# Kernel optimization log

Measured on AMD Instinct MI355X. Metric: run time of the kernel, lower is better.

The kernel has to match this reference:

```python
import jax, jax.numpy as jnp
import numpy as np

N_NODES = 50000
N_EDGES = 600000
IN_DIM = 128
HID_DIM = 128
OUT_DIM = 128
N_GRAPHS = 64


def _glorot(key, shape):
    lim = np.sqrt(6.0 / (shape[0] + shape[1]))
    return jax.random.uniform(key, shape, jnp.float32, -lim, lim)


def setup_inputs() -> dict:
    key = jax.random.key(0)
    ks = jax.random.split(key, 8)
    h = jax.random.normal(ks[0], (N_NODES, IN_DIM), jnp.float32)
    src = jax.random.randint(ks[1], (N_EDGES,), 0, N_NODES, jnp.int64)
    dst = jax.random.randint(ks[2], (N_EDGES,), 0, N_NODES, jnp.int64)
    graph_ids = jnp.sort(jax.random.randint(ks[3], (N_NODES,), 0, N_GRAPHS, jnp.int64))
    W1 = _glorot(ks[4], (IN_DIM, HID_DIM)); b1 = jnp.zeros((HID_DIM,), jnp.float32)
    W2 = _glorot(ks[5], (HID_DIM, HID_DIM)); b2 = jnp.zeros((HID_DIM,), jnp.float32)
    W3 = _glorot(ks[6], (HID_DIM, OUT_DIM)); b3 = jnp.zeros((OUT_DIM,), jnp.float32)
    return {"h": h, "src": src, "dst": dst, "graph_ids": graph_ids,
            "W1": W1, "b1": b1, "W2": W2, "b2": b2, "W3": W3, "b3": b3,
            "n_graphs": N_GRAPHS}


def _graph_conv(h, src, dst, norm_src, norm_dst, W, b):
    # DGL GraphConv, norm='both': D_dst^{-1/2} A^T D_src^{-1/2} h W + b
    m = h * norm_src[:, None]                                   # [N, d]
    agg = jax.ops.segment_sum(m[src], dst, num_segments=h.shape[0])  # [N, d]
    return (agg * norm_dst[:, None]) @ W + b


def reference(h, src, dst, graph_ids, W1, b1, W2, b2, W3, b3, n_graphs):
    n = h.shape[0]
    ones = jnp.ones((src.shape[0],), h.dtype)
    out_deg = jnp.clip(jax.ops.segment_sum(ones, src, num_segments=n), 1.0)
    in_deg = jnp.clip(jax.ops.segment_sum(ones, dst, num_segments=n), 1.0)
    norm_src = out_deg ** -0.5
    norm_dst = in_deg ** -0.5

    x = jax.nn.relu(_graph_conv(h, src, dst, norm_src, norm_dst, W1, b1))
    x = jax.nn.relu(_graph_conv(x, src, dst, norm_src, norm_dst, W2, b2))
    x = jax.nn.relu(_graph_conv(x, src, dst, norm_src, norm_dst, W3, b3))

    # dgl.mean_nodes: per-graph mean over nodes
    gsum = jax.ops.segment_sum(x, graph_ids, num_segments=n_graphs)          # [G, d]
    gcnt = jax.ops.segment_sum(jnp.ones((n,), x.dtype), graph_ids, num_segments=n_graphs)
    return gsum / jnp.clip(gcnt, 1.0)[:, None]
```

## Files before the change

kernel.cpp:

```cpp
#include <hip/hip_runtime.h>
#include <hip/hip_fp16.h>


#define DIM 128

typedef _Float16 half8 __attribute__((ext_vector_type(8)));
typedef float floatx4 __attribute__((ext_vector_type(4)));

#define HIST_R 4
#define HIST_S 64
#define NPR 12500
#define LDSW (NPR / 2)

__global__ __launch_bounds__(256) void k_hist(const int* __restrict__ src,
                                              const int* __restrict__ dst,
                                              unsigned* __restrict__ partial, int E) {
    __shared__ unsigned hist[LDSW];
    int b = blockIdx.x;
    int a = b / (HIST_R * HIST_S);
    int r = (b / HIST_S) % HIST_R;
    int s = b % HIST_S;
    const int* arr = a ? dst : src;
    for (int i = threadIdx.x; i < LDSW; i += 256) hist[i] = 0;
    __syncthreads();
    int chunk = (E + HIST_S - 1) / HIST_S;
    int e0 = s * chunk;
    int e1 = min(e0 + chunk, E);
    unsigned base = (unsigned)(r * NPR);
    for (int i = e0 + threadIdx.x; i < e1; i += 256) {
        unsigned n = (unsigned)arr[i] - base;
        if (n < NPR) atomicAdd(&hist[n >> 1], 1u << ((n & 1) * 16));
    }
    __syncthreads();
    unsigned* outp = partial + ((size_t)(a * HIST_R + r) * HIST_S + s) * LDSW;
    for (int i = threadIdx.x; i < LDSW; i += 256) outp[i] = hist[i];
}

__global__ void k_hist_merge(const unsigned* __restrict__ partial,
                             float* __restrict__ ns, float* __restrict__ nd,
                             int* __restrict__ inc, int N) {
    int t = blockIdx.x * blockDim.x + threadIdx.x;
    const int total_w = HIST_R * LDSW;
    if (t >= 2 * total_w) return;
    int a = t / total_w;
    int wg = t % total_w;
    int r = wg / LDSW;
    int w = wg % LDSW;
    const unsigned* p = partial + ((size_t)(a * HIST_R + r) * HIST_S) * LDSW + w;
    unsigned sum = 0;
#pragma unroll
    for (int s = 0; s < HIST_S; ++s) sum += p[(size_t)s * LDSW];
    int n0 = r * NPR + w * 2;
    int d0 = (int)(sum & 0xFFFFu);
    int d1 = (int)(sum >> 16);
    if (a == 0) {
        if (n0 < N)     ns[n0]     = rsqrtf(fmaxf((float)d0, 1.0f));
        if (n0 + 1 < N) ns[n0 + 1] = rsqrtf(fmaxf((float)d1, 1.0f));
    } else {
        if (n0 < N)     { nd[n0]     = rsqrtf(fmaxf((float)d0, 1.0f)); inc[n0]     = d0; }
        if (n0 + 1 < N) { nd[n0 + 1] = rsqrtf(fmaxf((float)d1, 1.0f)); inc[n0 + 1] = d1; }
    }
}

__global__ void k_scan_partial(const int* __restrict__ inc, int* __restrict__ bsum, int N) {
    __shared__ int s[256];
    int i = blockIdx.x * 256 + threadIdx.x;
    int t = threadIdx.x;
    s[t] = (i < N) ? inc[i] : 0;
    __syncthreads();
    for (int off = 128; off > 0; off >>= 1) {
        if (t < off) s[t] += s[t + off];
        __syncthreads();
    }
    if (t == 0) bsum[blockIdx.x] = s[0];
}

__global__ void k_scan_top(int* __restrict__ bsum, int nb) {
    __shared__ int s[256];
    int t = threadIdx.x;
    int v = (t < nb) ? bsum[t] : 0;
    s[t] = v;
    __syncthreads();
    for (int off = 1; off < 256; off <<= 1) {
        int u = (t >= off) ? s[t - off] : 0;
        __syncthreads();
        s[t] += u;
        __syncthreads();
    }
    if (t < nb) bsum[t] = s[t] - v;
}

__global__ void k_scan_write(const int* __restrict__ inc, const int* __restrict__ bsum,
                             int* __restrict__ row_ptr, int N) {
    __shared__ int s[256];
    int i = blockIdx.x * 256 + threadIdx.x;
    int t = threadIdx.x;
    int v = (i < N) ? inc[i] : 0;
    s[t] = v;
    __syncthreads();
    for (int off = 1; off < 256; off <<= 1) {
        int u = (t >= off) ? s[t - off] : 0;
        __syncthreads();
        s[t] += u;
        __syncthreads();
    }
    int ex = bsum[blockIdx.x] + s[t] - v;
    if (i < N) row_ptr[i] = ex;
    if (i == N - 1) row_ptr[N] = ex + v;
}

__global__ void k_cursor(const unsigned* __restrict__ partial, const int* __restrict__ row_ptr,
                         int* __restrict__ cur, int N) {
    int t = blockIdx.x * blockDim.x + threadIdx.x;
    if (t >= HIST_R * LDSW) return;
    int r = t / LDSW;
    int w = t % LDSW;
    int n0 = r * NPR + 2 * w;
    const unsigned* p = partial + ((size_t)(HIST_R + r) * HIST_S) * LDSW + w;
    int run0 = (n0 < N) ? row_ptr[n0] : 0;
    int run1 = (n0 + 1 < N) ? row_ptr[n0 + 1] : 0;
    int* c = cur + (size_t)r * HIST_S * NPR + 2 * w;
#pragma unroll
    for (int s = 0; s < HIST_S; ++s) {
        c[(size_t)s * NPR + 0] = run0;
        c[(size_t)s * NPR + 1] = run1;
        unsigned hv = p[(size_t)s * LDSW];
        run0 += (int)(hv & 0xFFFFu);
        run1 += (int)(hv >> 16);
    }
}

__global__ __launch_bounds__(256) void k_fill2(const int* __restrict__ src,
                                               const int* __restrict__ dst,
                                               const int* __restrict__ cur,
                                               int* __restrict__ csr, int E) {
    __shared__ int lcur[NPR];
    int r = blockIdx.x / HIST_S;
    int s = blockIdx.x % HIST_S;
    const int* cs = cur + (size_t)(r * HIST_S + s) * NPR;
    for (int i = threadIdx.x; i < NPR; i += 256) lcur[i] = cs[i];
    __syncthreads();
    int chunk = (E + HIST_S - 1) / HIST_S;
    int e0 = s * chunk;
    int e1 = min(e0 + chunk, E);
    unsigned base = (unsigned)(r * NPR);
    for (int i = e0 + threadIdx.x; i < e1; i += 256) {
        unsigned d = (unsigned)dst[i] - base;
        if (d < NPR) {
            int p = atomicAdd(&lcur[d], 1);
            csr[p] = src[i];
        }
    }
}

__global__ void k_h2half(const float4* __restrict__ h, const float* __restrict__ ns,
                         uint2* __restrict__ A, int N) {
    int i = blockIdx.x * blockDim.x + threadIdx.x;
    if (i < N * 32) {
        int n = i >> 5;
        float s = ns[n];
        float4 v = h[i];
        __half2 p0 = __floats2half2_rn(v.x * s, v.y * s);
        __half2 p1 = __floats2half2_rn(v.z * s, v.w * s);
        uint2 o;
        o.x = *(unsigned*)&p0;
        o.y = *(unsigned*)&p1;
        A[i] = o;
    }
}

__global__ void k_w2half(const float* __restrict__ W, _Float16* __restrict__ Wt) {
    int i = blockIdx.x * blockDim.x + threadIdx.x;
    int k = i >> 7;
    int n = i & 127;
    Wt[(size_t)n * DIM + k] = (_Float16)W[i];
}

__global__ void k_agg(const uint2* __restrict__ A, const int* __restrict__ row_ptr,
                      const int* __restrict__ csr, const float* __restrict__ nd,
                      uint2* __restrict__ Bh, int N) {
    int gtid = blockIdx.x * blockDim.x + threadIdx.x;
    int node = gtid >> 6;
    int lane = threadIdx.x & 63;
    if (node >= N) return;
    int e0 = row_ptr[node];
    int e1 = row_ptr[node + 1];
    int half = lane >> 5;
    int l8 = lane & 31;
    float ax = 0.f, ay = 0.f, az = 0.f, aw = 0.f;

    auto acc4 = [&](uint2 u) {
        __half2 p0 = *(__half2*)&u.x;
        __half2 p1 = *(__half2*)&u.y;
        float2 f0 = __half22float2(p0);
        float2 f1 = __half22float2(p1);
        ax += f0.x; ay += f0.y; az += f1.x; aw += f1.y;
    };

    int e = e0;
    for (; e + 8 <= e1; e += 8) {
        int s0 = csr[e + half];
        int s1 = csr[e + 2 + half];
        int s2 = csr[e + 4 + half];
        int s3 = csr[e + 6 + half];
        uint2 u0 = A[(size_t)s0 * 32 + l8];
        uint2 u1 = A[(size_t)s1 * 32 + l8];
        uint2 u2 = A[(size_t)s2 * 32 + l8];
        uint2 u3 = A[(size_t)s3 * 32 + l8];
        acc4(u0); acc4(u1); acc4(u2); acc4(u3);
    }
    for (; e + 2 <= e1; e += 2) {
        int s0 = csr[e + half];
        acc4(A[(size_t)s0 * 32 + l8]);
    }
    if (e < e1 && half == 0) {
        int s0 = csr[e];
        acc4(A[(size_t)s0 * 32 + l8]);
    }

    ax += __shfl_xor(ax, 32);
    ay += __shfl_xor(ay, 32);
    az += __shfl_xor(az, 32);
    aw += __shfl_xor(aw, 32);

    if (half == 0) {
        float scale = nd[node];
        __half2 p0 = __floats2half2_rn(ax * scale, ay * scale);
        __half2 p1 = __floats2half2_rn(az * scale, aw * scale);
        uint2 o;
        o.x = *(unsigned*)&p0;
        o.y = *(unsigned*)&p1;
        Bh[(size_t)node * 32 + l8] = o;
    }
}

template <bool HALF_OUT>
__global__ __launch_bounds__(256) void k_gemm_mfma(
    const _Float16* __restrict__ Bin, const _Float16* __restrict__ Wt,
    const float* __restrict__ bias, const float* __restrict__ ns,
    void* __restrict__ Xout, int N) {
    int tid = threadIdx.x;
    int wave = tid >> 6;
    int lane = tid & 63;
    int quad = lane >> 4;
    int l16 = lane & 15;
    int r0 = blockIdx.x * 64 + wave * 16;
    int arow = r0 + l16;

    half8 a[4];
#pragma unroll
    for (int q = 0; q < 4; ++q) {
        if (arow < N) {
            a[q] = *(const half8*)&Bin[(size_t)arow * DIM + q * 32 + quad * 8];
        } else {
            a[q] = half8{0, 0, 0, 0, 0, 0, 0, 0};
        }
    }

    floatx4 acc[8];
#pragma unroll
    for (int c = 0; c < 8; ++c) acc[c] = floatx4{0.f, 0.f, 0.f, 0.f};

#pragma unroll
    for (int c = 0; c < 8; ++c) {
#pragma unroll
        for (int q = 0; q < 4; ++q) {
            half8 b = *(const half8*)&Wt[(size_t)(c * 16 + l16) * DIM + q * 32 + quad * 8];
            acc[c] = __builtin_amdgcn_mfma_f32_16x16x32_f16(a[q], b, acc[c], 0, 0, 0);
        }
    }

    float bb[8];
#pragma unroll
    for (int c = 0; c < 8; ++c) bb[c] = bias[c * 16 + l16];

#pragma unroll
    for (int r = 0; r < 4; ++r) {
        int row = r0 + quad * 4 + r;
        if (row >= N) continue;
        float sr = HALF_OUT ? ns[row] : 1.0f;
#pragma unroll
        for (int c = 0; c < 8; ++c) {
            float v = fmaxf(acc[c][r] + bb[c], 0.0f);
            if (HALF_OUT) {
                ((_Float16*)Xout)[(size_t)row * DIM + c * 16 + l16] = (_Float16)(v * sr);
            } else {
                ((float*)Xout)[(size_t)row * DIM + c * 16 + l16] = v;
            }
        }
    }
}

#define POOL_NODES 32
__global__ void k_pool_partial(const float* __restrict__ X, const int* __restrict__ gid,
                               float* __restrict__ gsum, int* __restrict__ gcnt, int N) {
    int n0 = blockIdx.x * POOL_NODES;
    int d = threadIdx.x;
    int nend = min(n0 + POOL_NODES, N);
    float run = 0.0f;
    int cnt = 0;
    int curg = -1;
    for (int n = n0; n < nend; ++n) {
        int g = gid[n];
        if (g != curg) {
            if (cnt > 0) {
                atomicAdd(&gsum[curg * DIM + d], run);
                if (d == 0) atomicAdd(&gcnt[curg], cnt);
            }
            run = 0.0f; cnt = 0; curg = g;
        }
        run += X[(size_t)n * DIM + d];
        cnt++;
    }
    if (cnt > 0) {
        atomicAdd(&gsum[curg * DIM + d], run);
        if (d == 0) atomicAdd(&gcnt[curg], cnt);
    }
}

__global__ void k_finalize(const float* __restrict__ gsum, const int* __restrict__ gcnt,
                           float* __restrict__ out, int G) {
    int i = blockIdx.x * blockDim.x + threadIdx.x;
    if (i < G * DIM) {
        int g = i >> 7;
        float c = fmaxf((float)gcnt[g], 1.0f);
        out[i] = gsum[i] / c;
    }
}

extern "C" void kernel_launch(void* const* d_in, const int* in_sizes, int n_in,
                              void* d_out, int out_size, void* d_ws, size_t ws_size,
                              hipStream_t stream) {
    const float* h   = (const float*)d_in[0];
    const int*   src = (const int*)d_in[1];
    const int*   dst = (const int*)d_in[2];
    const int*   gid = (const int*)d_in[3];
    const float* W1  = (const float*)d_in[4];
    const float* b1  = (const float*)d_in[5];
    const float* W2  = (const float*)d_in[6];
    const float* b2  = (const float*)d_in[7];
    const float* W3  = (const float*)d_in[8];
    const float* b3  = (const float*)d_in[9];

    const int N = in_sizes[0] / DIM;
    const int E = in_sizes[1];
    const int G = 64;
    float* out = (float*)d_out;

    char* ws = (char*)d_ws;
    size_t off = 0;
    auto alloc = [&](size_t bytes) -> void* {
        void* p = ws + off;
        off += (bytes + 255) & ~(size_t)255;
        return p;
    };
    const int scanBlocks = (N + 255) / 256;
    uint2* Ah0     = (uint2*)alloc((size_t)N * DIM * 2);
    uint2* Ah1     = (uint2*)alloc((size_t)N * DIM * 2);
    uint2* Bh      = (uint2*)alloc((size_t)N * DIM * 2);
    float* X3      = (float*)alloc((size_t)N * DIM * 4);
    _Float16* Wt1  = (_Float16*)alloc((size_t)DIM * DIM * 2);
    _Float16* Wt2  = (_Float16*)alloc((size_t)DIM * DIM * 2);
    _Float16* Wt3  = (_Float16*)alloc((size_t)DIM * DIM * 2);
    float* ns      = (float*)alloc((size_t)N * 4);
    float* nd      = (float*)alloc((size_t)N * 4);
    int*   inc     = (int*)alloc((size_t)N * 4);
    unsigned* partial = (unsigned*)alloc((size_t)2 * HIST_R * HIST_S * LDSW * 4);
    int*   cur     = (int*)alloc((size_t)HIST_R * HIST_S * NPR * 4);
    int*   row_ptr = (int*)alloc((size_t)(N + 1) * 4);
    int*   csr     = (int*)alloc((size_t)E * 4);
    float* gsum    = (float*)alloc((size_t)G * DIM * 4);
    int*   gcnt    = (int*)alloc((size_t)G * 4);
    int*   bsum    = (int*)alloc((size_t)scanBlocks * 4);

    hipMemsetAsync(gsum, 0, (size_t)G * DIM * 4, stream);
    hipMemsetAsync(gcnt, 0, (size_t)G * 4, stream);

    k_hist<<<2 * HIST_R * HIST_S, 256, 0, stream>>>(src, dst, partial, E);
    int mergeThreads = 2 * HIST_R * LDSW;
    k_hist_merge<<<(mergeThreads + 255) / 256, 256, 0, stream>>>(partial, ns, nd, inc, N);

    k_scan_partial<<<scanBlocks, 256, 0, stream>>>(inc, bsum, N);
    k_scan_top<<<1, 256, 0, stream>>>(bsum, scanBlocks);
    k_scan_write<<<scanBlocks, 256, 0, stream>>>(inc, bsum, row_ptr, N);

    int curThreads = HIST_R * LDSW;
    k_cursor<<<(curThreads + 255) / 256, 256, 0, stream>>>(partial, row_ptr, cur, N);
    k_fill2<<<HIST_R * HIST_S, 256, 0, stream>>>(src, dst, cur, csr, E);

    k_w2half<<<64, 256, 0, stream>>>(W1, Wt1);
    k_w2half<<<64, 256, 0, stream>>>(W2, Wt2);
    k_w2half<<<64, 256, 0, stream>>>(W3, Wt3);

    int aggBlocks  = (N * 64 + 255) / 256;
    int gemmBlocks = (N + 63) / 64;

    k_h2half<<<(N * 32 + 255) / 256, 256, 0, stream>>>((const float4*)h, ns, Ah0, N);
    k_agg<<<aggBlocks, 256, 0, stream>>>(Ah0, row_ptr, csr, nd, Bh, N);
    k_gemm_mfma<true><<<gemmBlocks, 256, 0, stream>>>((const _Float16*)Bh, Wt1, b1, ns, Ah1, N);
    k_agg<<<aggBlocks, 256, 0, stream>>>(Ah1, row_ptr, csr, nd, Bh, N);
    k_gemm_mfma<true><<<gemmBlocks, 256, 0, stream>>>((const _Float16*)Bh, Wt2, b2, ns, Ah0, N);
    k_agg<<<aggBlocks, 256, 0, stream>>>(Ah0, row_ptr, csr, nd, Bh, N);
    k_gemm_mfma<false><<<gemmBlocks, 256, 0, stream>>>((const _Float16*)Bh, Wt3, b3, ns, X3, N);

    k_pool_partial<<<(N + POOL_NODES - 1) / POOL_NODES, 128, 0, stream>>>(X3, gid, gsum, gcnt, N);
    k_finalize<<<(G * DIM + 255) / 256, 256, 0, stream>>>(gsum, gcnt, out, G);
}
```

Baseline: 325.9 us.

## Batch gather loads in aggregation, store final layer in fp16, fuse weight conversions

The aggregation loop now fetches up to 16 neighbor indices per iteration and issues eight independent row gathers per half-wave before accumulating. Out-of-range slots are clamped and masked, which replaces the separate tail loops. The last GEMM now writes fp16 instead of fp32, halving its output traffic and the pooling kernel's reads. The three weight-transpose launches are merged into one. The trade-offs are extra gathers wasted on low-degree nodes, more register use, and reduced precision in the pooled output.

```diff
diff --git a/kernel.cpp b/kernel.cpp
--- a/kernel.cpp
+++ b/kernel.cpp
@@ -169,16 +169,24 @@
     }
 }
 
-__global__ void k_w2half(const float* __restrict__ W, _Float16* __restrict__ Wt) {
+__global__ void k_w2half3(const float* __restrict__ W1, const float* __restrict__ W2,
+                          const float* __restrict__ W3, _Float16* __restrict__ Wt1,
+                          _Float16* __restrict__ Wt2, _Float16* __restrict__ Wt3) {
     int i = blockIdx.x * blockDim.x + threadIdx.x;
-    int k = i >> 7;
-    int n = i & 127;
-    Wt[(size_t)n * DIM + k] = (_Float16)W[i];
-}
-
-__global__ void k_agg(const uint2* __restrict__ A, const int* __restrict__ row_ptr,
-                      const int* __restrict__ csr, const float* __restrict__ nd,
-                      uint2* __restrict__ Bh, int N) {
+    int j = i >> 14;
+    int local = i & 16383;
+    int k = local >> 7;
+    int n = local & 127;
+    const float* W = (j == 0) ? W1 : (j == 1) ? W2 : W3;
+    _Float16* Wt = (j == 0) ? Wt1 : (j == 1) ? Wt2 : Wt3;
+    Wt[(size_t)n * DIM + k] = (_Float16)W[local];
+}
+
+__global__ __launch_bounds__(256) void k_agg(const uint2* __restrict__ A,
+                                             const int* __restrict__ row_ptr,
+                                             const int* __restrict__ csr,
+                                             const float* __restrict__ nd,
+                                             uint2* __restrict__ Bh, int N) {
     int gtid = blockIdx.x * blockDim.x + threadIdx.x;
     int node = gtid >> 6;
     int lane = threadIdx.x & 63;
@@ -189,33 +197,29 @@
     int l8 = lane & 31;
     float ax = 0.f, ay = 0.f, az = 0.f, aw = 0.f;
 
-    auto acc4 = [&](uint2 u) {
-        __half2 p0 = *(__half2*)&u.x;
-        __half2 p1 = *(__half2*)&u.y;
-        float2 f0 = __half22float2(p0);
-        float2 f1 = __half22float2(p1);
-        ax += f0.x; ay += f0.y; az += f1.x; aw += f1.y;
-    };
-
-    int e = e0;
-    for (; e + 8 <= e1; e += 8) {
-        int s0 = csr[e + half];
-        int s1 = csr[e + 2 + half];
-        int s2 = csr[e + 4 + half];
-        int s3 = csr[e + 6 + half];
-        uint2 u0 = A[(size_t)s0 * 32 + l8];
-        uint2 u1 = A[(size_t)s1 * 32 + l8];
-        uint2 u2 = A[(size_t)s2 * 32 + l8];
-        uint2 u3 = A[(size_t)s3 * 32 + l8];
-        acc4(u0); acc4(u1); acc4(u2); acc4(u3);
-    }
-    for (; e + 2 <= e1; e += 2) {
-        int s0 = csr[e + half];
-        acc4(A[(size_t)s0 * 32 + l8]);
-    }
-    if (e < e1 && half == 0) {
-        int s0 = csr[e];
-        acc4(A[(size_t)s0 * 32 + l8]);
+    for (int base = e0; base < e1; base += 16) {
+        int idx[8];
+        uint2 u[8];
+#pragma unroll
+        for (int j = 0; j < 8; ++j) {
+            int ee = base + 2 * j + half;
+            idx[j] = csr[min(ee, e1 - 1)];
+        }
+#pragma unroll
+        for (int j = 0; j < 8; ++j) {
+            u[j] = A[(size_t)idx[j] * 32 + l8];
+        }
+#pragma unroll
+        for (int j = 0; j < 8; ++j) {
+            int ee = base + 2 * j + half;
+            if (ee < e1) {
+                __half2 p0 = *(__half2*)&u[j].x;
+                __half2 p1 = *(__half2*)&u[j].y;
+                float2 f0 = __half22float2(p0);
+                float2 f1 = __half22float2(p1);
+                ax += f0.x; ay += f0.y; az += f1.x; aw += f1.y;
+            }
+        }
     }
 
     ax += __shfl_xor(ax, 32);
@@ -234,11 +238,11 @@
     }
 }
 
-template <bool HALF_OUT>
+template <bool SCALE_NS>
 __global__ __launch_bounds__(256) void k_gemm_mfma(
     const _Float16* __restrict__ Bin, const _Float16* __restrict__ Wt,
     const float* __restrict__ bias, const float* __restrict__ ns,
-    void* __restrict__ Xout, int N) {
+    _Float16* __restrict__ Xout, int N) {
     int tid = threadIdx.x;
     int wave = tid >> 6;
     int lane = tid & 63;
@@ -278,21 +282,17 @@
     for (int r = 0; r < 4; ++r) {
         int row = r0 + quad * 4 + r;
         if (row >= N) continue;
-        float sr = HALF_OUT ? ns[row] : 1.0f;
+        float sr = SCALE_NS ? ns[row] : 1.0f;
 #pragma unroll
         for (int c = 0; c < 8; ++c) {
             float v = fmaxf(acc[c][r] + bb[c], 0.0f);
-            if (HALF_OUT) {
-                ((_Float16*)Xout)[(size_t)row * DIM + c * 16 + l16] = (_Float16)(v * sr);
-            } else {
-                ((float*)Xout)[(size_t)row * DIM + c * 16 + l16] = v;
-            }
+            Xout[(size_t)row * DIM + c * 16 + l16] = (_Float16)(v * sr);
         }
     }
 }
 
 #define POOL_NODES 32
-__global__ void k_pool_partial(const float* __restrict__ X, const int* __restrict__ gid,
+__global__ void k_pool_partial(const _Float16* __restrict__ X, const int* __restrict__ gid,
                                float* __restrict__ gsum, int* __restrict__ gcnt, int N) {
     int n0 = blockIdx.x * POOL_NODES;
     int d = threadIdx.x;
@@ -309,7 +309,7 @@
             }
             run = 0.0f; cnt = 0; curg = g;
         }
-        run += X[(size_t)n * DIM + d];
+        run += (float)X[(size_t)n * DIM + d];
         cnt++;
     }
     if (cnt > 0) {
@@ -358,7 +358,7 @@
     uint2* Ah0     = (uint2*)alloc((size_t)N * DIM * 2);
     uint2* Ah1     = (uint2*)alloc((size_t)N * DIM * 2);
     uint2* Bh      = (uint2*)alloc((size_t)N * DIM * 2);
-    float* X3      = (float*)alloc((size_t)N * DIM * 4);
+    _Float16* X3   = (_Float16*)alloc((size_t)N * DIM * 2);
     _Float16* Wt1  = (_Float16*)alloc((size_t)DIM * DIM * 2);
     _Float16* Wt2  = (_Float16*)alloc((size_t)DIM * DIM * 2);
     _Float16* Wt3  = (_Float16*)alloc((size_t)DIM * DIM * 2);
@@ -388,18 +388,16 @@
     k_cursor<<<(curThreads + 255) / 256, 256, 0, stream>>>(partial, row_ptr, cur, N);
     k_fill2<<<HIST_R * HIST_S, 256, 0, stream>>>(src, dst, cur, csr, E);
 
-    k_w2half<<<64, 256, 0, stream>>>(W1, Wt1);
-    k_w2half<<<64, 256, 0, stream>>>(W2, Wt2);
-    k_w2half<<<64, 256, 0, stream>>>(W3, Wt3);
+    k_w2half3<<<192, 256, 0, stream>>>(W1, W2, W3, Wt1, Wt2, Wt3);
 
     int aggBlocks  = (N * 64 + 255) / 256;
     int gemmBlocks = (N + 63) / 64;
 
     k_h2half<<<(N * 32 + 255) / 256, 256, 0, stream>>>((const float4*)h, ns, Ah0, N);
     k_agg<<<aggBlocks, 256, 0, stream>>>(Ah0, row_ptr, csr, nd, Bh, N);
-    k_gemm_mfma<true><<<gemmBlocks, 256, 0, stream>>>((const _Float16*)Bh, Wt1, b1, ns, Ah1, N);
+    k_gemm_mfma<true><<<gemmBlocks, 256, 0, stream>>>((const _Float16*)Bh, Wt1, b1, ns, (_Float16*)Ah1, N);
     k_agg<<<aggBlocks, 256, 0, stream>>>(Ah1, row_ptr, csr, nd, Bh, N);
-    k_gemm_mfma<true><<<gemmBlocks, 256, 0, stream>>>((const _Float16*)Bh, Wt2, b2, ns, Ah0, N);
+    k_gemm_mfma<true><<<gemmBlocks, 256, 0, stream>>>((const _Float16*)Bh, Wt2, b2, ns, (_Float16*)Ah0, N);
     k_agg<<<aggBlocks, 256, 0, stream>>>(Ah0, row_ptr, csr, nd, Bh, N);
     k_gemm_mfma<false><<<gemmBlocks, 256, 0, stream>>>((const _Float16*)Bh, Wt3, b3, ns, X3, N);
 
```

After: 317.8 us. 1.03x faster.
